# Kernel tuning notes

Hardware: AMD Instinct MI355X
Metric: run time of the kernel (lower is better)

The kernel has to match this reference:

```python
import jax, jax.numpy as jnp
import numpy as np

NUM_EXPERTS = 8
TOTAL_TOKENS = 16384
HIDDEN = 2048
FFN = 1408  # swiglu: h->2*FFN, chunk in half, silu(a)*b, FFN->h


def setup_inputs() -> dict:
    key = jax.random.key(0)
    k1, k2, k3 = jax.random.split(key, 3)
    permuted_hidden_states = jax.random.normal(k1, (TOTAL_TOKENS, HIDDEN), dtype=jnp.float32)
    # equal split so slice boundaries are static (cumsum boundaries of torch loop)
    num_tokens_per_expert = jnp.full((NUM_EXPERTS,), TOTAL_TOKENS // NUM_EXPERTS, dtype=jnp.int64)
    # per-expert weights: dense_h_to_4h (no bias, swiglu -> 2*FFN), dense_4h_to_h
    w1 = jax.random.normal(k2, (NUM_EXPERTS, HIDDEN, 2 * FFN), dtype=jnp.float32) * (1.0 / np.sqrt(HIDDEN))
    w2 = jax.random.normal(k3, (NUM_EXPERTS, FFN, HIDDEN), dtype=jnp.float32) * (1.0 / np.sqrt(FFN))
    return {
        "permuted_hidden_states": permuted_hidden_states,
        "num_tokens_per_expert": num_tokens_per_expert,
        "w1": w1,
        "w2": w2,
    }


def reference(permuted_hidden_states, num_tokens_per_expert, w1, w2):
    # Tokens are sorted by expert with equal counts -> static reshape replaces
    # the per-expert python slice loop; math identical to looping experts.
    E = w1.shape[0]
    T, H = permuted_hidden_states.shape
    h = permuted_hidden_states.reshape(E, T // E, H)          # [E, t, H]
    inter = jnp.einsum('eth,ehf->etf', h, w1)                 # [E, t, 2F]
    a, b = jnp.split(inter, 2, axis=-1)                        # swiglu chunks
    act = jax.nn.silu(a) * b                                   # [E, t, F]
    out = jnp.einsum('etf,efh->eth', act, w2)                 # [E, t, H]
    return out.reshape(T, H)
```

## Files before the change

kernel.cpp:

```cpp
#include <hip/hip_runtime.h>
#include <hip/hip_bf16.h>
#include <stdint.h>

#define TOKENS 16384
#define HIDDEN 2048
#define FFN    1408
#define NEXP   8
#define TPE    (TOKENS / NEXP)

typedef __attribute__((ext_vector_type(8))) short bf16x8;
typedef __attribute__((ext_vector_type(4))) float f32x4;

__device__ inline unsigned short f2bf(float f) {
    union { float f; unsigned u; } v; v.f = f;
    unsigned u = v.u;
    u += 0x7fffu + ((u >> 16) & 1u);
    return (unsigned short)(u >> 16);
}

__global__ void cast_x_kernel(const float* __restrict__ in, unsigned short* __restrict__ out) {
    size_t i = (size_t)blockIdx.x * blockDim.x + threadIdx.x;
    const float4* p = (const float4*)in;
    float4 v0 = p[2 * i];
    float4 v1 = p[2 * i + 1];
    bf16x8 o;
    o[0] = (short)f2bf(v0.x); o[1] = (short)f2bf(v0.y);
    o[2] = (short)f2bf(v0.z); o[3] = (short)f2bf(v0.w);
    o[4] = (short)f2bf(v1.x); o[5] = (short)f2bf(v1.y);
    o[6] = (short)f2bf(v1.z); o[7] = (short)f2bf(v1.w);
    *(bf16x8*)&out[8 * i] = o;
}

__global__ void transpose_cast_kernel(const float* __restrict__ in, unsigned short* __restrict__ out,
                                      int R, int C) {
    __shared__ float tile[64][65];
    const int e = blockIdx.z;
    const float* src = in + (size_t)e * R * C;
    unsigned short* dst = out + (size_t)e * R * C;
    const int tx = threadIdx.x & 63;
    const int ty = threadIdx.x >> 6;
    const int r0 = blockIdx.y * 64, c0 = blockIdx.x * 64;
#pragma unroll
    for (int p = 0; p < 16; ++p) {
        int r = p * 4 + ty;
        tile[r][tx] = src[(size_t)(r0 + r) * C + (c0 + tx)];
    }
    __syncthreads();
#pragma unroll
    for (int p = 0; p < 16; ++p) {
        int r = p * 4 + ty;
        dst[(size_t)(c0 + r) * R + (r0 + tx)] = f2bf(tile[tx][r]);
    }
}

#define BM 128
#define BN 128
#define BK 32

#define GLOAD_LDS16(g, l)                                                              \
    __builtin_amdgcn_global_load_lds((const __attribute__((address_space(1))) void*)(g), \
                                     (__attribute__((address_space(3))) void*)(l), 16, 0, 0)

__global__ __launch_bounds__(256, 2) void moe_gemm1_swiglu(
        const unsigned short* __restrict__ X,
        const unsigned short* __restrict__ W1T,
        unsigned short* __restrict__ ACT)
{
    const int e  = blockIdx.z;
    const int m0 = blockIdx.x * BM;
    const int n0 = blockIdx.y * BN;
    const int tid  = threadIdx.x;
    const int lane = tid & 63;
    const int w    = tid >> 6;
    const int wr = w >> 1, wc = w & 1;

    __shared__ __align__(16) unsigned short sA [BM * BK];
    __shared__ __align__(16) unsigned short sBa[BN * BK];
    __shared__ __align__(16) unsigned short sBb[BN * BK];
    char* sAc  = (char*)sA;
    char* sBac = (char*)sBa;
    char* sBbc = (char*)sBb;

    const unsigned short* Ag  = X   + ((size_t)e * TPE + m0) * HIDDEN;
    const unsigned short* Bag = W1T + ((size_t)e * (2 * FFN) + n0) * HIDDEN;
    const unsigned short* Bbg = W1T + ((size_t)e * (2 * FFN) + FFN + n0) * HIDDEN;

    f32x4 acc_a[4][4] = {};
    f32x4 acc_b[4][4] = {};

    const int crow = tid >> 2;
    const int kc8  = (tid & 3) * 8;
    const int ldsb0 = w * 1024;
    const int ldsb1 = w * 1024 + 4096;

    for (int kt = 0; kt < HIDDEN / BK; ++kt) {
        const int k0 = kt * BK;
        __syncthreads();
        {
            const unsigned short* g = Ag + (size_t)crow * HIDDEN + k0 + kc8;
            GLOAD_LDS16(g, sAc + ldsb0);
            GLOAD_LDS16(g + (size_t)64 * HIDDEN, sAc + ldsb1);
        }
        {
            const unsigned short* g = Bag + (size_t)crow * HIDDEN + k0 + kc8;
            GLOAD_LDS16(g, sBac + ldsb0);
            GLOAD_LDS16(g + (size_t)64 * HIDDEN, sBac + ldsb1);
        }
        {
            const unsigned short* g = Bbg + (size_t)crow * HIDDEN + k0 + kc8;
            GLOAD_LDS16(g, sBbc + ldsb0);
            GLOAD_LDS16(g + (size_t)64 * HIDDEN, sBbc + ldsb1);
        }
        __syncthreads();

        const int rrow = lane & 15;
        const int kb   = (lane >> 4) * 16;
        bf16x8 af[4], baf[4], bbf[4];
#pragma unroll
        for (int i = 0; i < 4; ++i)
            af[i] = *(const bf16x8*)(sAc + (wr * 64 + i * 16 + rrow) * (BK * 2) + kb);
#pragma unroll
        for (int j = 0; j < 4; ++j) {
            baf[j] = *(const bf16x8*)(sBac + (wc * 64 + j * 16 + rrow) * (BK * 2) + kb);
            bbf[j] = *(const bf16x8*)(sBbc + (wc * 64 + j * 16 + rrow) * (BK * 2) + kb);
        }
#pragma unroll
        for (int i = 0; i < 4; ++i)
#pragma unroll
            for (int j = 0; j < 4; ++j) {
                acc_a[i][j] = __builtin_amdgcn_mfma_f32_16x16x32_bf16(af[i], baf[j], acc_a[i][j], 0, 0, 0);
                acc_b[i][j] = __builtin_amdgcn_mfma_f32_16x16x32_bf16(af[i], bbf[j], acc_b[i][j], 0, 0, 0);
            }
    }

    const int rg   = lane >> 4;
    const int ccol = lane & 15;
    const size_t rowbase = (size_t)e * TPE + m0 + wr * 64;
#pragma unroll
    for (int i = 0; i < 4; ++i)
#pragma unroll
        for (int j = 0; j < 4; ++j)
#pragma unroll
            for (int r = 0; r < 4; ++r) {
                int row = i * 16 + rg * 4 + r;
                int col = n0 + wc * 64 + j * 16 + ccol;
                float a = acc_a[i][j][r];
                float b = acc_b[i][j][r];
                float s = (a / (1.0f + __expf(-a))) * b;
                ACT[(rowbase + row) * FFN + col] = f2bf(s);
            }
}

__global__ __launch_bounds__(256, 2) void moe_gemm2(
        const unsigned short* __restrict__ ACT,
        const unsigned short* __restrict__ W2T,
        float* __restrict__ OUT)
{
    const int e  = blockIdx.z;
    const int m0 = blockIdx.x * BM;
    const int n0 = blockIdx.y * BN;
    const int tid  = threadIdx.x;
    const int lane = tid & 63;
    const int w    = tid >> 6;
    const int wr = w >> 1, wc = w & 1;

    __shared__ __align__(16) unsigned short sA[BM * BK];
    __shared__ __align__(16) unsigned short sB[BN * BK];
    char* sAc = (char*)sA;
    char* sBc = (char*)sB;

    const unsigned short* Ag = ACT + ((size_t)e * TPE + m0) * FFN;
    const unsigned short* Bg = W2T + ((size_t)e * HIDDEN + n0) * FFN;

    f32x4 acc[4][4] = {};

    const int crow = tid >> 2;
    const int kc8  = (tid & 3) * 8;
    const int ldsb0 = w * 1024;
    const int ldsb1 = w * 1024 + 4096;

    for (int kt = 0; kt < FFN / BK; ++kt) {
        const int k0 = kt * BK;
        __syncthreads();
        {
            const unsigned short* g = Ag + (size_t)crow * FFN + k0 + kc8;
            GLOAD_LDS16(g, sAc + ldsb0);
            GLOAD_LDS16(g + (size_t)64 * FFN, sAc + ldsb1);
        }
        {
            const unsigned short* g = Bg + (size_t)crow * FFN + k0 + kc8;
            GLOAD_LDS16(g, sBc + ldsb0);
            GLOAD_LDS16(g + (size_t)64 * FFN, sBc + ldsb1);
        }
        __syncthreads();

        const int rrow = lane & 15;
        const int kb   = (lane >> 4) * 16;
        bf16x8 af[4], bf[4];
#pragma unroll
        for (int i = 0; i < 4; ++i)
            af[i] = *(const bf16x8*)(sAc + (wr * 64 + i * 16 + rrow) * (BK * 2) + kb);
#pragma unroll
        for (int j = 0; j < 4; ++j)
            bf[j] = *(const bf16x8*)(sBc + (wc * 64 + j * 16 + rrow) * (BK * 2) + kb);
#pragma unroll
        for (int i = 0; i < 4; ++i)
#pragma unroll
            for (int j = 0; j < 4; ++j)
                acc[i][j] = __builtin_amdgcn_mfma_f32_16x16x32_bf16(af[i], bf[j], acc[i][j], 0, 0, 0);
    }

    const int rg   = lane >> 4;
    const int ccol = lane & 15;
    const size_t rowbase = (size_t)e * TPE + m0 + wr * 64;
#pragma unroll
    for (int i = 0; i < 4; ++i)
#pragma unroll
        for (int j = 0; j < 4; ++j)
#pragma unroll
            for (int r = 0; r < 4; ++r) {
                int row = i * 16 + rg * 4 + r;
                int col = n0 + wc * 64 + j * 16 + ccol;
                OUT[(rowbase + row) * HIDDEN + col] = acc[i][j][r];
            }
}

extern "C" void kernel_launch(void* const* d_in, const int* in_sizes, int n_in,
                              void* d_out, int out_size, void* d_ws, size_t ws_size,
                              hipStream_t stream) {
    const float* x  = (const float*)d_in[0];
    const float* w1 = (const float*)d_in[2];
    const float* w2 = (const float*)d_in[3];
    float* out = (float*)d_out;

    char* ws = (char*)d_ws;
    unsigned short* xb  = (unsigned short*)(ws);
    unsigned short* w1T = (unsigned short*)(ws + 67108864);
    unsigned short* w2T = (unsigned short*)(ws + 159383552);
    unsigned short* act = (unsigned short*)(ws + 205520896);

    cast_x_kernel<<<dim3((TOKENS * HIDDEN) / (256 * 8)), 256, 0, stream>>>(x, xb);
    transpose_cast_kernel<<<dim3((2 * FFN) / 64, HIDDEN / 64, NEXP), 256, 0, stream>>>(w1, w1T, HIDDEN, 2 * FFN);
    transpose_cast_kernel<<<dim3(HIDDEN / 64, FFN / 64, NEXP), 256, 0, stream>>>(w2, w2T, FFN, HIDDEN);

    moe_gemm1_swiglu<<<dim3(TPE / BM, FFN / BN, NEXP), 256, 0, stream>>>(xb, w1T, act);

    moe_gemm2<<<dim3(TPE / BM, HIDDEN / BN, NEXP), 256, 0, stream>>>(act, w2T, out);
}
```

Before: 809.3 us.

## Replace MoE GEMMs with 256x256 8-wave double-buffered pipelined kernel, split SwiGLU

Replaces both 128x128 BK=32 GEMM kernels with a templated 256x256 tile, 512-thread kernel. It double-buffers K=64 stages in LDS with an XOR swizzle and interleaves global-to-LDS loads with MFMA quarters, using raw barriers, waitcnt and setprio. The fused SwiGLU epilogue is removed: GEMM1 now writes a bf16 intermediate of width 2*FFN, and a separate elementwise kernel applies SwiGLU, reusing the x buffer for the activation output. The aim is higher MFMA utilization through larger tiles and overlapped loads, at the cost of an extra bf16 round-trip through global memory and an added rounding of the pre-activation values.

Result: faster. 724.3 us (-10.5%).

```diff
diff --git a/kernel.cpp b/kernel.cpp
--- a/kernel.cpp
+++ b/kernel.cpp
@@ -16,6 +16,9 @@
     unsigned u = v.u;
     u += 0x7fffu + ((u >> 16) & 1u);
     return (unsigned short)(u >> 16);
+}
+__device__ inline float bf2f(unsigned short u) {
+    union { unsigned u; float f; } v; v.u = ((unsigned)u) << 16; return v.f;
 }
 
 __global__ void cast_x_kernel(const float* __restrict__ in, unsigned short* __restrict__ out) {
@@ -53,176 +56,173 @@
     }
 }
 
-#define BM 128
-#define BN 128
-#define BK 32
+__global__ void swiglu_kernel(const unsigned short* __restrict__ inter, unsigned short* __restrict__ act) {
+    int i = blockIdx.x * 256 + threadIdx.x;
+    int t = i / (FFN / 8);
+    int f = (i % (FFN / 8)) * 8;
+    bf16x8 a8 = *(const bf16x8*)&inter[(size_t)t * (2 * FFN) + f];
+    bf16x8 b8 = *(const bf16x8*)&inter[(size_t)t * (2 * FFN) + FFN + f];
+    bf16x8 o;
+#pragma unroll
+    for (int j = 0; j < 8; ++j) {
+        float a = bf2f((unsigned short)a8[j]);
+        float b = bf2f((unsigned short)b8[j]);
+        float s = (a / (1.0f + __expf(-a))) * b;
+        o[j] = (short)f2bf(s);
+    }
+    *(bf16x8*)&act[(size_t)t * FFN + f] = o;
+}
+
+__device__ inline void store_c(float* p, float v) { *p = v; }
+__device__ inline void store_c(unsigned short* p, float v) { *p = f2bf(v); }
 
 #define GLOAD_LDS16(g, l)                                                              \
     __builtin_amdgcn_global_load_lds((const __attribute__((address_space(1))) void*)(g), \
                                      (__attribute__((address_space(3))) void*)(l), 16, 0, 0)
 
-__global__ __launch_bounds__(256, 2) void moe_gemm1_swiglu(
-        const unsigned short* __restrict__ X,
-        const unsigned short* __restrict__ W1T,
-        unsigned short* __restrict__ ACT)
+#define BAR()    __builtin_amdgcn_s_barrier()
+#define CFENCE() asm volatile("" ::: "memory")
+#define LGKM0()  asm volatile("s_waitcnt lgkmcnt(0)" ::: "memory")
+#define VMC4()   asm volatile("s_waitcnt vmcnt(4)" ::: "memory")
+#define VMC0()   asm volatile("s_waitcnt vmcnt(0)" ::: "memory")
+
+#define STAGE(slot_, op_, half_, tk_) do {                                              \
+    const unsigned short* gb_ = ((op_) ? Bg : Ag)                                       \
+        + (size_t)((half_) * 128 + srow) * K + (tk_) * 64 + scol;                       \
+    char* db_ = L + (slot_) * 65536 + (op_) * 32768 + (half_) * 16384 + (w << 10);      \
+    GLOAD_LDS16(gb_, db_);                                                              \
+    GLOAD_LDS16(gb_ + (size_t)64 * K, db_ + 8192);                                      \
+  } while (0)
+
+#define LOAD_A(slot_, mh_) do {                                                         \
+    const char* Ab_ = L + (slot_) * 65536 + (mh_) * 16384 + aoff;                       \
+    af[0][0] = *(const bf16x8*)(Ab_ + colb0);        af[0][1] = *(const bf16x8*)(Ab_ + colb1); \
+    af[1][0] = *(const bf16x8*)(Ab_ + 2048 + colb0); af[1][1] = *(const bf16x8*)(Ab_ + 2048 + colb1); \
+    af[2][0] = *(const bf16x8*)(Ab_ + 4096 + colb0); af[2][1] = *(const bf16x8*)(Ab_ + 4096 + colb1); \
+    af[3][0] = *(const bf16x8*)(Ab_ + 6144 + colb0); af[3][1] = *(const bf16x8*)(Ab_ + 6144 + colb1); \
+  } while (0)
+
+#define LOAD_B(slot_, nh_) do {                                                         \
+    const char* Bb_ = L + (slot_) * 65536 + 32768 + (nh_) * 16384 + boff;               \
+    bfr[(nh_)*2][0]   = *(const bf16x8*)(Bb_ + colb0);        bfr[(nh_)*2][1]   = *(const bf16x8*)(Bb_ + colb1); \
+    bfr[(nh_)*2+1][0] = *(const bf16x8*)(Bb_ + 2048 + colb0); bfr[(nh_)*2+1][1] = *(const bf16x8*)(Bb_ + 2048 + colb1); \
+  } while (0)
+
+#define MFMA_Q(mh_, nh_) do {                                                           \
+    _Pragma("unroll")                                                                   \
+    for (int kk2 = 0; kk2 < 2; ++kk2)                                                   \
+    _Pragma("unroll")                                                                   \
+    for (int mm = 0; mm < 4; ++mm)                                                      \
+    _Pragma("unroll")                                                                   \
+    for (int nn = 0; nn < 2; ++nn)                                                      \
+        acc[(mh_)*4+mm][(nh_)*2+nn] = __builtin_amdgcn_mfma_f32_16x16x32_bf16(          \
+            af[mm][kk2], bfr[(nh_)*2+nn][kk2], acc[(mh_)*4+mm][(nh_)*2+nn], 0, 0, 0);   \
+  } while (0)
+
+#define PRIO1() __builtin_amdgcn_s_setprio(1)
+#define PRIO0() __builtin_amdgcn_s_setprio(0)
+
+template <int K, int NCOLS, int NBLK, typename OutT>
+__global__ __launch_bounds__(512, 2) void gemm8p(
+        const unsigned short* __restrict__ Abase,
+        const unsigned short* __restrict__ Bbase,
+        OutT* __restrict__ Cbase)
 {
-    const int e  = blockIdx.z;
-    const int m0 = blockIdx.x * BM;
-    const int n0 = blockIdx.y * BN;
-    const int tid  = threadIdx.x;
-    const int lane = tid & 63;
-    const int w    = tid >> 6;
-    const int wr = w >> 1, wc = w & 1;
-
-    __shared__ __align__(16) unsigned short sA [BM * BK];
-    __shared__ __align__(16) unsigned short sBa[BN * BK];
-    __shared__ __align__(16) unsigned short sBb[BN * BK];
-    char* sAc  = (char*)sA;
-    char* sBac = (char*)sBa;
-    char* sBbc = (char*)sBb;
-
-    const unsigned short* Ag  = X   + ((size_t)e * TPE + m0) * HIDDEN;
-    const unsigned short* Bag = W1T + ((size_t)e * (2 * FFN) + n0) * HIDDEN;
-    const unsigned short* Bbg = W1T + ((size_t)e * (2 * FFN) + FFN + n0) * HIDDEN;
-
-    f32x4 acc_a[4][4] = {};
-    f32x4 acc_b[4][4] = {};
-
-    const int crow = tid >> 2;
-    const int kc8  = (tid & 3) * 8;
-    const int ldsb0 = w * 1024;
-    const int ldsb1 = w * 1024 + 4096;
-
-    for (int kt = 0; kt < HIDDEN / BK; ++kt) {
-        const int k0 = kt * BK;
-        __syncthreads();
-        {
-            const unsigned short* g = Ag + (size_t)crow * HIDDEN + k0 + kc8;
-            GLOAD_LDS16(g, sAc + ldsb0);
-            GLOAD_LDS16(g + (size_t)64 * HIDDEN, sAc + ldsb1);
+    constexpr int NT = K / 64;
+    constexpr int NITER = NT / 2;
+
+    const int bid = blockIdx.x;
+    const int e   = bid & 7;
+    const int rem = bid >> 3;
+    const int nb  = rem >> 3;
+    const int mb  = rem & 7;
+    const int m0 = mb * 256, n0 = nb * 256;
+
+    const unsigned short* Ag = Abase + ((size_t)e * 2048 + m0) * K;
+    const unsigned short* Bg = Bbase + ((size_t)e * (NBLK * 256) + n0) * K;
+
+    const int tid = threadIdx.x, lane = tid & 63, w = tid >> 6;
+    const int wr = w >> 2, wc = w & 3;
+
+    __shared__ __align__(16) unsigned short lds[2][2][2][8192];
+    char* L = (char*)lds;
+
+    const int srow = (w << 3) + (lane >> 3);
+    const int scol = ((lane & 7) ^ (lane >> 3)) << 3;
+
+    const int arow = lane & 15;
+    const int colb0 = (((lane >> 4) << 4)) ^ ((lane & 7) << 4);
+    const int colb1 = (64 | ((lane >> 4) << 4)) ^ ((lane & 7) << 4);
+    const int aoff = (wr * 64 + arow) * 128;
+    const int boff = (wc * 32 + arow) * 128;
+
+    f32x4 acc[8][4] = {};
+    bf16x8 af[4][2], bfr[4][2];
+
+    STAGE(0, 0, 0, 0); STAGE(0, 1, 0, 0);
+    STAGE(0, 0, 1, 0); STAGE(0, 1, 1, 0);
+    STAGE(1, 0, 0, 1); STAGE(1, 1, 0, 1);
+    VMC4();
+    BAR(); CFENCE();
+
+    for (int it = 0; it < NITER; ++it) {
+        const int t = 2 * it;
+        const bool more = (it + 1) < NITER;
+
+        LOAD_A(0, 0); LOAD_B(0, 0);
+        STAGE(1, 0, 1, t + 1);
+        BAR(); CFENCE(); LGKM0();
+        PRIO1(); MFMA_Q(0, 0); PRIO0();
+        BAR(); CFENCE();
+        LOAD_B(0, 1);
+        STAGE(1, 1, 1, t + 1);
+        BAR(); CFENCE(); LGKM0();
+        PRIO1(); MFMA_Q(0, 1); PRIO0();
+        BAR(); CFENCE();
+        LOAD_A(0, 1);
+        if (more) STAGE(0, 0, 0, t + 2);
+        BAR(); CFENCE(); LGKM0();
+        PRIO1(); MFMA_Q(1, 0); PRIO0();
+        BAR(); CFENCE();
+        if (more) STAGE(0, 1, 0, t + 2);
+        BAR(); CFENCE();
+        PRIO1(); MFMA_Q(1, 1); PRIO0();
+        if (more) VMC4(); else VMC0();
+        BAR(); CFENCE();
+        LOAD_A(1, 0); LOAD_B(1, 0);
+        if (more) STAGE(0, 0, 1, t + 2);
+        BAR(); CFENCE(); LGKM0();
+        PRIO1(); MFMA_Q(0, 0); PRIO0();
+        BAR(); CFENCE();
+        LOAD_B(1, 1);
+        if (more) STAGE(0, 1, 1, t + 2);
+        BAR(); CFENCE(); LGKM0();
+        PRIO1(); MFMA_Q(0, 1); PRIO0();
+        BAR(); CFENCE();
+        LOAD_A(1, 1);
+        if (more) STAGE(1, 0, 0, t + 3);
+        BAR(); CFENCE(); LGKM0();
+        PRIO1(); MFMA_Q(1, 0); PRIO0();
+        BAR(); CFENCE();
+        if (more) STAGE(1, 1, 0, t + 3);
+        BAR(); CFENCE();
+        PRIO1(); MFMA_Q(1, 1); PRIO0();
+        if (more) VMC4(); else VMC0();
+        BAR(); CFENCE();
+    }
+
+    OutT* Cg = Cbase + ((size_t)e * 2048 + m0) * NCOLS + n0;
+#pragma unroll
+    for (int m = 0; m < 8; ++m) {
+        const int rbase = (m >> 2) * 128 + wr * 64 + (m & 3) * 16 + (lane >> 4) * 4;
+#pragma unroll
+        for (int n = 0; n < 4; ++n) {
+            const int c = (n >> 1) * 128 + wc * 32 + (n & 1) * 16 + (lane & 15);
+#pragma unroll
+            for (int r = 0; r < 4; ++r)
+                store_c(&Cg[(size_t)(rbase + r) * NCOLS + c], acc[m][n][r]);
         }
-        {
-            const unsigned short* g = Bag + (size_t)crow * HIDDEN + k0 + kc8;
-            GLOAD_LDS16(g, sBac + ldsb0);
-            GLOAD_LDS16(g + (size_t)64 * HIDDEN, sBac + ldsb1);
-        }
-        {
-            const unsigned short* g = Bbg + (size_t)crow * HIDDEN + k0 + kc8;
-            GLOAD_LDS16(g, sBbc + ldsb0);
-            GLOAD_LDS16(g + (size_t)64 * HIDDEN, sBbc + ldsb1);
-        }
-        __syncthreads();
-
-        const int rrow = lane & 15;
-        const int kb   = (lane >> 4) * 16;
-        bf16x8 af[4], baf[4], bbf[4];
-#pragma unroll
-        for (int i = 0; i < 4; ++i)
-            af[i] = *(const bf16x8*)(sAc + (wr * 64 + i * 16 + rrow) * (BK * 2) + kb);
-#pragma unroll
-        for (int j = 0; j < 4; ++j) {
-            baf[j] = *(const bf16x8*)(sBac + (wc * 64 + j * 16 + rrow) * (BK * 2) + kb);
-            bbf[j] = *(const bf16x8*)(sBbc + (wc * 64 + j * 16 + rrow) * (BK * 2) + kb);
-        }
-#pragma unroll
-        for (int i = 0; i < 4; ++i)
-#pragma unroll
-            for (int j = 0; j < 4; ++j) {
-                acc_a[i][j] = __builtin_amdgcn_mfma_f32_16x16x32_bf16(af[i], baf[j], acc_a[i][j], 0, 0, 0);
-                acc_b[i][j] = __builtin_amdgcn_mfma_f32_16x16x32_bf16(af[i], bbf[j], acc_b[i][j], 0, 0, 0);
-            }
-    }
-
-    const int rg   = lane >> 4;
-    const int ccol = lane & 15;
-    const size_t rowbase = (size_t)e * TPE + m0 + wr * 64;
-#pragma unroll
-    for (int i = 0; i < 4; ++i)
-#pragma unroll
-        for (int j = 0; j < 4; ++j)
-#pragma unroll
-            for (int r = 0; r < 4; ++r) {
-                int row = i * 16 + rg * 4 + r;
-                int col = n0 + wc * 64 + j * 16 + ccol;
-                float a = acc_a[i][j][r];
-                float b = acc_b[i][j][r];
-                float s = (a / (1.0f + __expf(-a))) * b;
-                ACT[(rowbase + row) * FFN + col] = f2bf(s);
-            }
-}
-
-__global__ __launch_bounds__(256, 2) void moe_gemm2(
-        const unsigned short* __restrict__ ACT,
-        const unsigned short* __restrict__ W2T,
-        float* __restrict__ OUT)
-{
-    const int e  = blockIdx.z;
-    const int m0 = blockIdx.x * BM;
-    const int n0 = blockIdx.y * BN;
-    const int tid  = threadIdx.x;
-    const int lane = tid & 63;
-    const int w    = tid >> 6;
-    const int wr = w >> 1, wc = w & 1;
-
-    __shared__ __align__(16) unsigned short sA[BM * BK];
-    __shared__ __align__(16) unsigned short sB[BN * BK];
-    char* sAc = (char*)sA;
-    char* sBc = (char*)sB;
-
-    const unsigned short* Ag = ACT + ((size_t)e * TPE + m0) * FFN;
-    const unsigned short* Bg = W2T + ((size_t)e * HIDDEN + n0) * FFN;
-
-    f32x4 acc[4][4] = {};
-
-    const int crow = tid >> 2;
-    const int kc8  = (tid & 3) * 8;
-    const int ldsb0 = w * 1024;
-    const int ldsb1 = w * 1024 + 4096;
-
-    for (int kt = 0; kt < FFN / BK; ++kt) {
-        const int k0 = kt * BK;
-        __syncthreads();
-        {
-            const unsigned short* g = Ag + (size_t)crow * FFN + k0 + kc8;
-            GLOAD_LDS16(g, sAc + ldsb0);
-            GLOAD_LDS16(g + (size_t)64 * FFN, sAc + ldsb1);
-        }
-        {
-            const unsigned short* g = Bg + (size_t)crow * FFN + k0 + kc8;
-            GLOAD_LDS16(g, sBc + ldsb0);
-            GLOAD_LDS16(g + (size_t)64 * FFN, sBc + ldsb1);
-        }
-        __syncthreads();
-
-        const int rrow = lane & 15;
-        const int kb   = (lane >> 4) * 16;
-        bf16x8 af[4], bf[4];
-#pragma unroll
-        for (int i = 0; i < 4; ++i)
-            af[i] = *(const bf16x8*)(sAc + (wr * 64 + i * 16 + rrow) * (BK * 2) + kb);
-#pragma unroll
-        for (int j = 0; j < 4; ++j)
-            bf[j] = *(const bf16x8*)(sBc + (wc * 64 + j * 16 + rrow) * (BK * 2) + kb);
-#pragma unroll
-        for (int i = 0; i < 4; ++i)
-#pragma unroll
-            for (int j = 0; j < 4; ++j)
-                acc[i][j] = __builtin_amdgcn_mfma_f32_16x16x32_bf16(af[i], bf[j], acc[i][j], 0, 0, 0);
-    }
-
-    const int rg   = lane >> 4;
-    const int ccol = lane & 15;
-    const size_t rowbase = (size_t)e * TPE + m0 + wr * 64;
-#pragma unroll
-    for (int i = 0; i < 4; ++i)
-#pragma unroll
-        for (int j = 0; j < 4; ++j)
-#pragma unroll
-            for (int r = 0; r < 4; ++r) {
-                int row = i * 16 + rg * 4 + r;
-                int col = n0 + wc * 64 + j * 16 + ccol;
-                OUT[(rowbase + row) * HIDDEN + col] = acc[i][j][r];
-            }
+    }
 }
 
 extern "C" void kernel_launch(void* const* d_in, const int* in_sizes, int n_in,
@@ -234,16 +234,17 @@
     float* out = (float*)d_out;
 
     char* ws = (char*)d_ws;
-    unsigned short* xb  = (unsigned short*)(ws);
-    unsigned short* w1T = (unsigned short*)(ws + 67108864);
-    unsigned short* w2T = (unsigned short*)(ws + 159383552);
-    unsigned short* act = (unsigned short*)(ws + 205520896);
+    unsigned short* xb    = (unsigned short*)(ws);
+    unsigned short* w1T   = (unsigned short*)(ws + 67108864);
+    unsigned short* w2T   = (unsigned short*)(ws + 159383552);
+    unsigned short* inter = (unsigned short*)(ws + 205520896);
+    unsigned short* act   = (unsigned short*)(ws);
 
     cast_x_kernel<<<dim3((TOKENS * HIDDEN) / (256 * 8)), 256, 0, stream>>>(x, xb);
     transpose_cast_kernel<<<dim3((2 * FFN) / 64, HIDDEN / 64, NEXP), 256, 0, stream>>>(w1, w1T, HIDDEN, 2 * FFN);
     transpose_cast_kernel<<<dim3(HIDDEN / 64, FFN / 64, NEXP), 256, 0, stream>>>(w2, w2T, FFN, HIDDEN);
 
-    moe_gemm1_swiglu<<<dim3(TPE / BM, FFN / BN, NEXP), 256, 0, stream>>>(xb, w1T, act);
-
-    moe_gemm2<<<dim3(TPE / BM, HIDDEN / BN, NEXP), 256, 0, stream>>>(act, w2T, out);
-}
+    gemm8p<HIDDEN, 2 * FFN, 11, unsigned short><<<8 * 8 * 11, 512, 0, stream>>>(xb, w1T, inter);
+    swiglu_kernel<<<(TOKENS * (FFN / 8)) / 256, 256, 0, stream>>>(inter, act);
+    gemm8p<FFN, HIDDEN, 8, float><<<8 * 8 * 8, 512, 0, stream>>>(act, w2T, out);
+}
```
